# Performance work log

Hardware: AMD Instinct MI355X
Metric: run time of the kernel (lower is better)

Reference implementation:

```python
import jax, jax.numpy as jnp
import numpy as np

H = 20  # hidden size (hard-coded in the module)

def setup_inputs() -> dict:
    key = jax.random.key(0)
    ks = jax.random.split(key, 7)
    B, T = 4096, 1000
    s = 1.0 / np.sqrt(H)  # torch default init bound for RNN/Linear
    x = jax.random.normal(ks[0], (B, T, 1), dtype=jnp.float32)
    W_ih = jax.random.uniform(ks[1], (H, 1), jnp.float32, -s, s)
    W_hh = jax.random.uniform(ks[2], (H, H), jnp.float32, -s, s)
    b_ih = jax.random.uniform(ks[3], (H,), jnp.float32, -s, s)
    b_hh = jax.random.uniform(ks[4], (H,), jnp.float32, -s, s)
    fc_w = jax.random.uniform(ks[5], (1, H), jnp.float32, -s, s)
    fc_b = jax.random.uniform(ks[6], (1,), jnp.float32, -s, s)
    return {"x": x, "W_ih": W_ih, "W_hh": W_hh, "b_ih": b_ih,
            "b_hh": b_hh, "fc_w": fc_w, "fc_b": fc_b}

def reference(x, W_ih, W_hh, b_ih, b_hh, fc_w, fc_b):
    # x: [B, T, 1] -> time-major [T, B, 1] for scan
    B = x.shape[0]
    xt = jnp.swapaxes(x, 0, 1)
    # precompute input projection for all timesteps: [T, B, H]
    xproj = jnp.einsum('tbi,hi->tbh', xt, W_ih) + b_ih + b_hh
    h0 = jnp.zeros((B, H), dtype=x.dtype)
    def step(h, xp_t):
        h_new = jax.nn.relu(xp_t + h @ W_hh.T)
        return h_new, None
    h_last, _ = jax.lax.scan(step, h0, xproj)
    # only the last hidden state feeds the head: fc1(rnn_out[:, -1, :])
    out = h_last @ fc_w.T + fc_b  # [B, 1]
    return out
```

## Files before the change

### kernel.cpp

```cpp
#include <hip/hip_runtime.h>


#define TT 1000

typedef float v2f __attribute__((ext_vector_type(2)));

struct Col { v2f p01, p23; float v4; };

#define PIN(v)  asm volatile("" : "+v"(v))
__device__ __forceinline__ void pinc(Col& c) {
    PIN(c.p01); PIN(c.p23); PIN(c.v4);
}
__device__ __forceinline__ void keepc(const Col& c) {
    asm volatile("" :: "v"(c.p01), "v"(c.p23), "v"(c.v4));
}

template <int CTRL>
__device__ __forceinline__ float dpp_f(float v) {
    return __int_as_float(__builtin_amdgcn_update_dpp(
        0, __float_as_int(v), CTRL, 0xF, 0xF, true));
}

#define QP_XOR1 0xB1
#define QP_XOR2 0x4E
#define ROR4   0x124
#define ROR8   0x128

template <int C1, int C2>
__device__ __forceinline__ void step(float xt, v2f& h01, v2f& h23, float& h4,
                                     const Col& wc0, const Col& wc1,
                                     const Col& wc2, const Col& wc3,
                                     const Col& wc4,
                                     const Col& wih, const Col& bias) {
    const v2f xs = {xt, xt};
    v2f  A01 = __builtin_elementwise_fma(xs, wih.p01, bias.p01);
    v2f  A23 = __builtin_elementwise_fma(xs, wih.p23, bias.p23);
    float a4 = __builtin_fmaf(xt, wih.v4, bias.v4);

#define KCOL(hk, wc) {                                             \
        const v2f hs = {hk, hk};                                   \
        A01 = __builtin_elementwise_fma(hs, (wc).p01, A01);        \
        A23 = __builtin_elementwise_fma(hs, (wc).p23, A23);        \
        a4  = __builtin_fmaf(hk, (wc).v4, a4); }
    KCOL(h01.x, wc0) KCOL(h01.y, wc1) KCOL(h23.x, wc2) KCOL(h23.y, wc3) KCOL(h4, wc4)
#undef KCOL

    float b0 = A01.x, b1 = A01.y, b2 = A23.x, b3 = A23.y, b4 = a4;
    {
        float t0 = dpp_f<C1>(b0), t1 = dpp_f<C1>(b1), t2 = dpp_f<C1>(b2),
              t3 = dpp_f<C1>(b3), t4 = dpp_f<C1>(b4);
        b0 += t0; b1 += t1; b2 += t2; b3 += t3; b4 += t4;
    }
    {
        float t0 = dpp_f<C2>(b0), t1 = dpp_f<C2>(b1), t2 = dpp_f<C2>(b2),
              t3 = dpp_f<C2>(b3), t4 = dpp_f<C2>(b4);
        b0 += t0; b1 += t1; b2 += t2; b3 += t3; b4 += t4;
    }

    const v2f z = {0.f, 0.f};
    v2f r01 = {b0, b1};
    v2f r23 = {b2, b3};
    h01 = __builtin_elementwise_max(r01, z);
    h23 = __builtin_elementwise_max(r23, z);
    h4  = fmaxf(b4, 0.f);
}

__global__ void
__attribute__((amdgpu_flat_work_group_size(64, 64), amdgpu_waves_per_eu(1, 1)))
rnn_pk_kernel(const float* __restrict__ x,
              const float* __restrict__ W_ih,
              const float* __restrict__ W_hh,
              const float* __restrict__ b_ih,
              const float* __restrict__ b_hh,
              const float* __restrict__ fc_w,
              const float* __restrict__ fc_b,
              float* __restrict__ out) {
    const int tid = blockIdx.x * 64 + threadIdx.x;
    const int b   = tid >> 4;
    const int gl  = tid & 15;
    const int a   = gl >> 2;
    const int bq  = gl & 3;

    Col we0, we1, we2, we3, we4;
    Col wo0, wo1, wo2, wo3, wo4;
#define LOADC(wk, k, rbase, cbase)                                            \
    { (wk).p01 = (v2f){ W_hh[((rbase) + 0) * 20 + (cbase) + (k)],             \
                        W_hh[((rbase) + 1) * 20 + (cbase) + (k)] };           \
      (wk).p23 = (v2f){ W_hh[((rbase) + 2) * 20 + (cbase) + (k)],             \
                        W_hh[((rbase) + 3) * 20 + (cbase) + (k)] };           \
      (wk).v4  =        W_hh[((rbase) + 4) * 20 + (cbase) + (k)]; }
    LOADC(we0, 0, a * 5, bq * 5) LOADC(we1, 1, a * 5, bq * 5)
    LOADC(we2, 2, a * 5, bq * 5) LOADC(we3, 3, a * 5, bq * 5)
    LOADC(we4, 4, a * 5, bq * 5)
    LOADC(wo0, 0, bq * 5, a * 5) LOADC(wo1, 1, bq * 5, a * 5)
    LOADC(wo2, 2, bq * 5, a * 5) LOADC(wo3, 3, bq * 5, a * 5)
    LOADC(wo4, 4, bq * 5, a * 5)
#undef LOADC

    const bool eact = (bq == 0);
    const bool oact = (a == 0);
    Col wie, bie, wio, bio;
#define LOADIB(wv, bv, base, act)                                             \
    { const float* pw = W_ih + (base);                                        \
      const float* p1 = b_ih + (base);                                        \
      const float* p2 = b_hh + (base);                                        \
      (wv).p01 = (v2f){ (act) ? pw[0] : 0.f, (act) ? pw[1] : 0.f };           \
      (wv).p23 = (v2f){ (act) ? pw[2] : 0.f, (act) ? pw[3] : 0.f };           \
      (wv).v4  =        (act) ? pw[4] : 0.f;                                  \
      (bv).p01 = (v2f){ (act) ? (p1[0] + p2[0]) : 0.f,                        \
                        (act) ? (p1[1] + p2[1]) : 0.f };                      \
      (bv).p23 = (v2f){ (act) ? (p1[2] + p2[2]) : 0.f,                        \
                        (act) ? (p1[3] + p2[3]) : 0.f };                      \
      (bv).v4  =        (act) ? (p1[4] + p2[4]) : 0.f; }
    LOADIB(wie, bie, a * 5,  eact)
    LOADIB(wio, bio, bq * 5, oact)
#undef LOADIB

    pinc(we0); pinc(we1); pinc(we2); pinc(we3); pinc(we4);
    pinc(wo0); pinc(wo1); pinc(wo2); pinc(wo3); pinc(wo4);
    pinc(wie); pinc(bie); pinc(wio); pinc(bio);

    v2f h01 = {0.f, 0.f}, h23 = {0.f, 0.f};
    float h4 = 0.f;

    const float* __restrict__ xb = x + (size_t)b * TT;

#define LOAD10(P, off)                                  \
    P##0 = *(const float4*)(xb + (off));                \
    P##1 = *(const float4*)(xb + (off) + 4);            \
    P##2 = *(const float4*)(xb + (off) + 8);            \
    P##3 = *(const float4*)(xb + (off) + 12);           \
    P##4 = *(const float4*)(xb + (off) + 16);           \
    P##5 = *(const float4*)(xb + (off) + 20);           \
    P##6 = *(const float4*)(xb + (off) + 24);           \
    P##7 = *(const float4*)(xb + (off) + 28);           \
    P##8 = *(const float4*)(xb + (off) + 32);           \
    P##9 = *(const float4*)(xb + (off) + 36);

#define STEP_E(xv) step<QP_XOR1, QP_XOR2>(xv, h01, h23, h4, we0, we1, we2, we3, we4, wie, bie);
#define STEP_O(xv) step<ROR4,    ROR8   >(xv, h01, h23, h4, wo0, wo1, wo2, wo3, wo4, wio, bio);
#define RUN4(Q)  STEP_E(Q.x) STEP_O(Q.y) STEP_E(Q.z) STEP_O(Q.w)
#define RUN40(P) RUN4(P##0) RUN4(P##1) RUN4(P##2) RUN4(P##3) RUN4(P##4) \
                 RUN4(P##5) RUN4(P##6) RUN4(P##7) RUN4(P##8) RUN4(P##9)

    float4 A0, A1, A2, A3, A4, A5, A6, A7, A8, A9;
    float4 B0, B1, B2, B3, B4, B5, B6, B7, B8, B9;
    LOAD10(A, 0)
    LOAD10(B, 40)

    for (int it = 0; it < 12; ++it) {
        const int base = it * 80;
        const int nb = (it < 11) ? base + 120 : 960;

        RUN40(A)
        LOAD10(A, base + 80)
        RUN40(B)
        LOAD10(B, nb)
    }
    RUN40(A)

#undef RUN40
#undef RUN4
#undef STEP_E
#undef STEP_O
#undef LOAD10

    keepc(we0); keepc(we1); keepc(we2); keepc(we3); keepc(we4);
    keepc(wo0); keepc(wo1); keepc(wo2); keepc(wo3); keepc(wo4);
    keepc(wie); keepc(bie); keepc(wio); keepc(bio);

    float dot;
    {
        const float* pf = fc_w + bq * 5;
        float f0 = oact ? pf[0] : 0.f, f1 = oact ? pf[1] : 0.f;
        float f2 = oact ? pf[2] : 0.f, f3 = oact ? pf[3] : 0.f;
        float f4 = oact ? pf[4] : 0.f;
        dot = h01.x * f0;
        dot = __builtin_fmaf(h01.y, f1, dot);
        dot = __builtin_fmaf(h23.x, f2, dot);
        dot = __builtin_fmaf(h23.y, f3, dot);
        dot = __builtin_fmaf(h4,    f4, dot);
    }
    dot += __shfl_xor(dot, 1, 16);
    dot += __shfl_xor(dot, 2, 16);
    dot += __shfl_xor(dot, 4, 16);
    dot += __shfl_xor(dot, 8, 16);

    if (gl == 0)
        out[b] = dot + fc_b[0];
}

extern "C" void kernel_launch(void* const* d_in, const int* in_sizes, int n_in,
                              void* d_out, int out_size, void* d_ws, size_t ws_size,
                              hipStream_t stream) {
    const float* x    = (const float*)d_in[0];
    const float* W_ih = (const float*)d_in[1];
    const float* W_hh = (const float*)d_in[2];
    const float* b_ih = (const float*)d_in[3];
    const float* b_hh = (const float*)d_in[4];
    const float* fc_w = (const float*)d_in[5];
    const float* fc_b = (const float*)d_in[6];
    float* out = (float*)d_out;

    const int block = 64;
    const int grid  = (4096 * 16) / block;
    rnn_pk_kernel<<<grid, block, 0, stream>>>(x, W_ih, W_hh, b_ih, b_hh,
                                              fc_w, fc_b, out);
}
```

Measured before the change: 147.1 us.

## Process two batch rows per lane group using packed FMA across batches

```diff
diff --git a/kernel.cpp b/kernel.cpp
--- a/kernel.cpp
+++ b/kernel.cpp
@@ -5,14 +5,16 @@
 
 typedef float v2f __attribute__((ext_vector_type(2)));
 
-struct Col { v2f p01, p23; float v4; };
+struct C5 { v2f c0, c1, c2, c3, c4; };
+
+#define SPL(s) ((v2f){(s), (s)})
 
 #define PIN(v)  asm volatile("" : "+v"(v))
-__device__ __forceinline__ void pinc(Col& c) {
-    PIN(c.p01); PIN(c.p23); PIN(c.v4);
-}
-__device__ __forceinline__ void keepc(const Col& c) {
-    asm volatile("" :: "v"(c.p01), "v"(c.p23), "v"(c.v4));
+__device__ __forceinline__ void pinc(C5& c) {
+    PIN(c.c0); PIN(c.c1); PIN(c.c2); PIN(c.c3); PIN(c.c4);
+}
+__device__ __forceinline__ void keepc(const C5& c) {
+    asm volatile("" :: "v"(c.c0), "v"(c.c1), "v"(c.c2), "v"(c.c3), "v"(c.c4));
 }
 
 template <int CTRL>
@@ -26,48 +28,50 @@
 #define ROR4   0x124
 #define ROR8   0x128
 
+template <int C>
+__device__ __forceinline__ v2f fold_pair(v2f a) {
+    float lo = a.x, hi = a.y;
+    float tl = dpp_f<C>(lo), th = dpp_f<C>(hi);
+    lo += tl; hi += th;
+    return (v2f){lo, hi};
+}
+
 template <int C1, int C2>
-__device__ __forceinline__ void step(float xt, v2f& h01, v2f& h23, float& h4,
-                                     const Col& wc0, const Col& wc1,
-                                     const Col& wc2, const Col& wc3,
-                                     const Col& wc4,
-                                     const Col& wih, const Col& bias) {
-    const v2f xs = {xt, xt};
-    v2f  A01 = __builtin_elementwise_fma(xs, wih.p01, bias.p01);
-    v2f  A23 = __builtin_elementwise_fma(xs, wih.p23, bias.p23);
-    float a4 = __builtin_fmaf(xt, wih.v4, bias.v4);
-
-#define KCOL(hk, wc) {                                             \
-        const v2f hs = {hk, hk};                                   \
-        A01 = __builtin_elementwise_fma(hs, (wc).p01, A01);        \
-        A23 = __builtin_elementwise_fma(hs, (wc).p23, A23);        \
-        a4  = __builtin_fmaf(hk, (wc).v4, a4); }
-    KCOL(h01.x, wc0) KCOL(h01.y, wc1) KCOL(h23.x, wc2) KCOL(h23.y, wc3) KCOL(h4, wc4)
+__device__ __forceinline__ void step(v2f xp, C5& h,
+                                     const C5& w0, const C5& w1, const C5& w2,
+                                     const C5& w3, const C5& w4,
+                                     const C5& wih, const C5& bias) {
+    v2f a0 = __builtin_elementwise_fma(xp, wih.c0, bias.c0);
+    v2f a1 = __builtin_elementwise_fma(xp, wih.c1, bias.c1);
+    v2f a2 = __builtin_elementwise_fma(xp, wih.c2, bias.c2);
+    v2f a3 = __builtin_elementwise_fma(xp, wih.c3, bias.c3);
+    v2f a4 = __builtin_elementwise_fma(xp, wih.c4, bias.c4);
+
+#define KCOL(hp, wc)                                          \
+    a0 = __builtin_elementwise_fma(hp, (wc).c0, a0);          \
+    a1 = __builtin_elementwise_fma(hp, (wc).c1, a1);          \
+    a2 = __builtin_elementwise_fma(hp, (wc).c2, a2);          \
+    a3 = __builtin_elementwise_fma(hp, (wc).c3, a3);          \
+    a4 = __builtin_elementwise_fma(hp, (wc).c4, a4);
+    KCOL(h.c0, w0) KCOL(h.c1, w1) KCOL(h.c2, w2) KCOL(h.c3, w3) KCOL(h.c4, w4)
 #undef KCOL
 
-    float b0 = A01.x, b1 = A01.y, b2 = A23.x, b3 = A23.y, b4 = a4;
-    {
-        float t0 = dpp_f<C1>(b0), t1 = dpp_f<C1>(b1), t2 = dpp_f<C1>(b2),
-              t3 = dpp_f<C1>(b3), t4 = dpp_f<C1>(b4);
-        b0 += t0; b1 += t1; b2 += t2; b3 += t3; b4 += t4;
-    }
-    {
-        float t0 = dpp_f<C2>(b0), t1 = dpp_f<C2>(b1), t2 = dpp_f<C2>(b2),
-              t3 = dpp_f<C2>(b3), t4 = dpp_f<C2>(b4);
-        b0 += t0; b1 += t1; b2 += t2; b3 += t3; b4 += t4;
-    }
+    a0 = fold_pair<C1>(a0); a1 = fold_pair<C1>(a1); a2 = fold_pair<C1>(a2);
+    a3 = fold_pair<C1>(a3); a4 = fold_pair<C1>(a4);
+    a0 = fold_pair<C2>(a0); a1 = fold_pair<C2>(a1); a2 = fold_pair<C2>(a2);
+    a3 = fold_pair<C2>(a3); a4 = fold_pair<C2>(a4);
 
     const v2f z = {0.f, 0.f};
-    v2f r01 = {b0, b1};
-    v2f r23 = {b2, b3};
-    h01 = __builtin_elementwise_max(r01, z);
-    h23 = __builtin_elementwise_max(r23, z);
-    h4  = fmaxf(b4, 0.f);
+    h.c0 = __builtin_elementwise_max(a0, z);
+    h.c1 = __builtin_elementwise_max(a1, z);
+    h.c2 = __builtin_elementwise_max(a2, z);
+    h.c3 = __builtin_elementwise_max(a3, z);
+    h.c4 = __builtin_elementwise_max(a4, z);
 }
 
 __global__ void
 __attribute__((amdgpu_flat_work_group_size(64, 64), amdgpu_waves_per_eu(1, 1)))
-rnn_pk_kernel(const float* __restrict__ x,
+rnn_bp_kernel(const float* __restrict__ x,
               const float* __restrict__ W_ih,
               const float* __restrict__ W_hh,
               const float* __restrict__ b_ih,
@@ -76,19 +80,19 @@
               const float* __restrict__ fc_b,
               float* __restrict__ out) {
     const int tid = blockIdx.x * 64 + threadIdx.x;
-    const int b   = tid >> 4;
+    const int p   = tid >> 4;
     const int gl  = tid & 15;
     const int a   = gl >> 2;
     const int bq  = gl & 3;
 
-    Col we0, we1, we2, we3, we4;
-    Col wo0, wo1, wo2, wo3, wo4;
+    C5 we0, we1, we2, we3, we4;
+    C5 wo0, wo1, wo2, wo3, wo4;
 #define LOADC(wk, k, rbase, cbase)                                            \
-    { (wk).p01 = (v2f){ W_hh[((rbase) + 0) * 20 + (cbase) + (k)],             \
-                        W_hh[((rbase) + 1) * 20 + (cbase) + (k)] };           \
-      (wk).p23 = (v2f){ W_hh[((rbase) + 2) * 20 + (cbase) + (k)],             \
-                        W_hh[((rbase) + 3) * 20 + (cbase) + (k)] };           \
-      (wk).v4  =        W_hh[((rbase) + 4) * 20 + (cbase) + (k)]; }
+    { (wk).c0 = SPL(W_hh[((rbase) + 0) * 20 + (cbase) + (k)]);                \
+      (wk).c1 = SPL(W_hh[((rbase) + 1) * 20 + (cbase) + (k)]);                \
+      (wk).c2 = SPL(W_hh[((rbase) + 2) * 20 + (cbase) + (k)]);                \
+      (wk).c3 = SPL(W_hh[((rbase) + 3) * 20 + (cbase) + (k)]);                \
+      (wk).c4 = SPL(W_hh[((rbase) + 4) * 20 + (cbase) + (k)]); }
     LOADC(we0, 0, a * 5, bq * 5) LOADC(we1, 1, a * 5, bq * 5)
     LOADC(we2, 2, a * 5, bq * 5) LOADC(we3, 3, a * 5, bq * 5)
     LOADC(we4, 4, a * 5, bq * 5)
@@ -99,19 +103,21 @@
 
     const bool eact = (bq == 0);
     const bool oact = (a == 0);
-    Col wie, bie, wio, bio;
+    C5 wie, bie, wio, bio;
 #define LOADIB(wv, bv, base, act)                                             \
     { const float* pw = W_ih + (base);                                        \
       const float* p1 = b_ih + (base);                                        \
       const float* p2 = b_hh + (base);                                        \
-      (wv).p01 = (v2f){ (act) ? pw[0] : 0.f, (act) ? pw[1] : 0.f };           \
-      (wv).p23 = (v2f){ (act) ? pw[2] : 0.f, (act) ? pw[3] : 0.f };           \
-      (wv).v4  =        (act) ? pw[4] : 0.f;                                  \
-      (bv).p01 = (v2f){ (act) ? (p1[0] + p2[0]) : 0.f,                        \
-                        (act) ? (p1[1] + p2[1]) : 0.f };                      \
-      (bv).p23 = (v2f){ (act) ? (p1[2] + p2[2]) : 0.f,                        \
-                        (act) ? (p1[3] + p2[3]) : 0.f };                      \
-      (bv).v4  =        (act) ? (p1[4] + p2[4]) : 0.f; }
+      (wv).c0 = SPL((act) ? pw[0] : 0.f);                                     \
+      (wv).c1 = SPL((act) ? pw[1] : 0.f);                                     \
+      (wv).c2 = SPL((act) ? pw[2] : 0.f);                                     \
+      (wv).c3 = SPL((act) ? pw[3] : 0.f);                                     \
+      (wv).c4 = SPL((act) ? pw[4] : 0.f);                                     \
+      (bv).c0 = SPL((act) ? (p1[0] + p2[0]) : 0.f);                           \
+      (bv).c1 = SPL((act) ? (p1[1] + p2[1]) : 0.f);                           \
+      (bv).c2 = SPL((act) ? (p1[2] + p2[2]) : 0.f);                           \
+      (bv).c3 = SPL((act) ? (p1[3] + p2[3]) : 0.f);                           \
+      (bv).c4 = SPL((act) ? (p1[4] + p2[4]) : 0.f); }
     LOADIB(wie, bie, a * 5,  eact)
     LOADIB(wio, bio, bq * 5, oact)
 #undef LOADIB
@@ -120,74 +126,80 @@
     pinc(wo0); pinc(wo1); pinc(wo2); pinc(wo3); pinc(wo4);
     pinc(wie); pinc(bie); pinc(wio); pinc(bio);
 
-    v2f h01 = {0.f, 0.f}, h23 = {0.f, 0.f};
-    float h4 = 0.f;
-
-    const float* __restrict__ xb = x + (size_t)b * TT;
-
-#define LOAD10(P, off)                                  \
-    P##0 = *(const float4*)(xb + (off));                \
-    P##1 = *(const float4*)(xb + (off) + 4);            \
-    P##2 = *(const float4*)(xb + (off) + 8);            \
-    P##3 = *(const float4*)(xb + (off) + 12);           \
-    P##4 = *(const float4*)(xb + (off) + 16);           \
-    P##5 = *(const float4*)(xb + (off) + 20);           \
-    P##6 = *(const float4*)(xb + (off) + 24);           \
-    P##7 = *(const float4*)(xb + (off) + 28);           \
-    P##8 = *(const float4*)(xb + (off) + 32);           \
-    P##9 = *(const float4*)(xb + (off) + 36);
-
-#define STEP_E(xv) step<QP_XOR1, QP_XOR2>(xv, h01, h23, h4, we0, we1, we2, we3, we4, wie, bie);
-#define STEP_O(xv) step<ROR4,    ROR8   >(xv, h01, h23, h4, wo0, wo1, wo2, wo3, wo4, wio, bio);
-#define RUN4(Q)  STEP_E(Q.x) STEP_O(Q.y) STEP_E(Q.z) STEP_O(Q.w)
-#define RUN40(P) RUN4(P##0) RUN4(P##1) RUN4(P##2) RUN4(P##3) RUN4(P##4) \
-                 RUN4(P##5) RUN4(P##6) RUN4(P##7) RUN4(P##8) RUN4(P##9)
-
-    float4 A0, A1, A2, A3, A4, A5, A6, A7, A8, A9;
-    float4 B0, B1, B2, B3, B4, B5, B6, B7, B8, B9;
-    LOAD10(A, 0)
-    LOAD10(B, 40)
-
-    for (int it = 0; it < 12; ++it) {
-        const int base = it * 80;
-        const int nb = (it < 11) ? base + 120 : 960;
-
-        RUN40(A)
-        LOAD10(A, base + 80)
-        RUN40(B)
-        LOAD10(B, nb)
+    C5 h;
+    h.c0 = SPL(0.f); h.c1 = SPL(0.f); h.c2 = SPL(0.f);
+    h.c3 = SPL(0.f); h.c4 = SPL(0.f);
+
+    const float* __restrict__ xb0 = x + (size_t)(2 * p) * TT;
+    const float* __restrict__ xb1 = xb0 + TT;
+
+#define LOAD5(P0, P1, P2, P3, P4, src, off)             \
+    P0 = *(const float4*)((src) + (off));               \
+    P1 = *(const float4*)((src) + (off) + 4);           \
+    P2 = *(const float4*)((src) + (off) + 8);           \
+    P3 = *(const float4*)((src) + (off) + 12);          \
+    P4 = *(const float4*)((src) + (off) + 16);
+
+#define STEP_E(xp) step<QP_XOR1, QP_XOR2>(xp, h, we0, we1, we2, we3, we4, wie, bie);
+#define STEP_O(xp) step<ROR4,    ROR8   >(xp, h, wo0, wo1, wo2, wo3, wo4, wio, bio);
+#define RUN4(Qa, Qc)                              \
+    STEP_E(((v2f){Qa.x, Qc.x}))                   \
+    STEP_O(((v2f){Qa.y, Qc.y}))                   \
+    STEP_E(((v2f){Qa.z, Qc.z}))                   \
+    STEP_O(((v2f){Qa.w, Qc.w}))
+#define RUN20(PA0, PA1, PA2, PA3, PA4, PC0, PC1, PC2, PC3, PC4)  \
+    RUN4(PA0, PC0) RUN4(PA1, PC1) RUN4(PA2, PC2) RUN4(PA3, PC3) RUN4(PA4, PC4)
+
+    float4 A0, A1, A2, A3, A4, B0, B1, B2, B3, B4;
+    float4 Ca0, Ca1, Ca2, Ca3, Ca4, D0, D1, D2, D3, D4;
+    LOAD5(A0, A1, A2, A3, A4, xb0, 0)
+    LOAD5(Ca0, Ca1, Ca2, Ca3, Ca4, xb1, 0)
+    LOAD5(B0, B1, B2, B3, B4, xb0, 20)
+    LOAD5(D0, D1, D2, D3, D4, xb1, 20)
+
+    for (int it = 0; it < 25; ++it) {
+        const int base = it * 40;
+        const int na = (it < 24) ? base + 40 : 920;
+        const int nb = (it < 24) ? base + 60 : 940;
+
+        RUN20(A0, A1, A2, A3, A4, Ca0, Ca1, Ca2, Ca3, Ca4)
+        LOAD5(A0, A1, A2, A3, A4, xb0, na)
+        LOAD5(Ca0, Ca1, Ca2, Ca3, Ca4, xb1, na)
+        RUN20(B0, B1, B2, B3, B4, D0, D1, D2, D3, D4)
+        LOAD5(B0, B1, B2, B3, B4, xb0, nb)
+        LOAD5(D0, D1, D2, D3, D4, xb1, nb)
     }
-    RUN40(A)
-
-#undef RUN40
+
+#undef RUN20
 #undef RUN4
 #undef STEP_E
 #undef STEP_O
-#undef LOAD10
+#undef LOAD5
 
     keepc(we0); keepc(we1); keepc(we2); keepc(we3); keepc(we4);
     keepc(wo0); keepc(wo1); keepc(wo2); keepc(wo3); keepc(wo4);
     keepc(wie); keepc(bie); keepc(wio); keepc(bio);
 
-    float dot;
+    v2f dotp = {0.f, 0.f};
     {
         const float* pf = fc_w + bq * 5;
-        float f0 = oact ? pf[0] : 0.f, f1 = oact ? pf[1] : 0.f;
-        float f2 = oact ? pf[2] : 0.f, f3 = oact ? pf[3] : 0.f;
-        float f4 = oact ? pf[4] : 0.f;
-        dot = h01.x * f0;
-        dot = __builtin_fmaf(h01.y, f1, dot);
-        dot = __builtin_fmaf(h23.x, f2, dot);
-        dot = __builtin_fmaf(h23.y, f3, dot);
-        dot = __builtin_fmaf(h4,    f4, dot);
+        dotp = __builtin_elementwise_fma(h.c0, SPL(oact ? pf[0] : 0.f), dotp);
+        dotp = __builtin_elementwise_fma(h.c1, SPL(oact ? pf[1] : 0.f), dotp);
+        dotp = __builtin_elementwise_fma(h.c2, SPL(oact ? pf[2] : 0.f), dotp);
+        dotp = __builtin_elementwise_fma(h.c3, SPL(oact ? pf[3] : 0.f), dotp);
+        dotp = __builtin_elementwise_fma(h.c4, SPL(oact ? pf[4] : 0.f), dotp);
     }
-    dot += __shfl_xor(dot, 1, 16);
-    dot += __shfl_xor(dot, 2, 16);
-    dot += __shfl_xor(dot, 4, 16);
-    dot += __shfl_xor(dot, 8, 16);
-
-    if (gl == 0)
-        out[b] = dot + fc_b[0];
+    float d0 = dotp.x, d1 = dotp.y;
+    d0 += __shfl_xor(d0, 1, 16); d1 += __shfl_xor(d1, 1, 16);
+    d0 += __shfl_xor(d0, 2, 16); d1 += __shfl_xor(d1, 2, 16);
+    d0 += __shfl_xor(d0, 4, 16); d1 += __shfl_xor(d1, 4, 16);
+    d0 += __shfl_xor(d0, 8, 16); d1 += __shfl_xor(d1, 8, 16);
+
+    if (gl == 0) {
+        const float fb = fc_b[0];
+        out[2 * p]     = d0 + fb;
+        out[2 * p + 1] = d1 + fb;
+    }
 }
 
 extern "C" void kernel_launch(void* const* d_in, const int* in_sizes, int n_in,
@@ -203,7 +215,7 @@
     float* out = (float*)d_out;
 
     const int block = 64;
-    const int grid  = (4096 * 16) / block;
-    rnn_pk_kernel<<<grid, block, 0, stream>>>(x, W_ih, W_hh, b_ih, b_hh,
+    const int grid  = (2048 * 16) / block;
+    rnn_bp_kernel<<<grid, block, 0, stream>>>(x, W_ih, W_hh, b_ih, b_hh,
                                               fc_w, fc_b, out);
 }
```

New measurement: 218.3 us. 1.48x slower.
